# Performance work log

Hardware: AMD Instinct MI355X
Metric: run time of the kernel (lower is better)

## Reference

```python
import jax, jax.numpy as jnp
import numpy as np


def setup_inputs() -> dict:
    key = jax.random.key(0)
    k1, k2 = jax.random.split(key)
    N, I, J, K = 256, 32, 32, 256
    x = jax.random.normal(k1, (N, I, K), dtype=jnp.float32)
    z = jax.random.normal(k2, (N, J, K), dtype=jnp.float32)
    return {"x": x, "z": z}


def reference(x, z):
    # Original torch code loops over batch rolls; rolling only permutes the set
    # over which log_softmax (a permutation-invariant logsumexp) is taken, and
    # index 0 of the roll stack is always the diagonal pair (x[n], z[n]).
    # So it is exactly a symmetric InfoNCE over the full pairwise score matrix.
    J = z.shape[1]
    # Full pairwise token-level similarity: [N_x, N_z, I, J]
    sim = jnp.einsum('aik,bjk->abij', x, z)
    # score(x_a, z_b) = sum_{i,j} softmax_i(sim)*sim / J
    w = jax.nn.softmax(sim, axis=2) * sim
    S = w.sum(axis=(2, 3)) / J  # [N_x, N_z]
    diag = jnp.diagonal(S)
    # loss_x[n] = -log_softmax over x-candidates (axis 0) at the diagonal
    loss_x = jax.nn.logsumexp(S, axis=0) - diag
    # loss_z[n] = -log_softmax over z-candidates (axis 1) at the diagonal
    loss_z = jax.nn.logsumexp(S, axis=1) - diag
    loss = loss_x + loss_z
    return loss.mean()  # reduction='mean'
```

## Files before the change

### kernel.cpp

```cpp
#include <hip/hip_runtime.h>
#include <hip/hip_bf16.h>
#include <hip/hip_fp16.h>
#include <stdint.h>


typedef __attribute__((ext_vector_type(8))) short short8;
typedef __attribute__((ext_vector_type(16))) float float16;
typedef __attribute__((ext_vector_type(8))) int int8v;
typedef __attribute__((ext_vector_type(4))) int int4v;

typedef const __attribute__((address_space(1))) unsigned int* gptr_as1;
typedef __attribute__((address_space(3))) unsigned int* lptr_as3;

#define NTOK 256
#define KDIM 256

__device__ __forceinline__ unsigned short f2bf(float f) {
    unsigned int u = __float_as_uint(f);
    unsigned int r = (u + 0x7fffu + ((u >> 16) & 1u)) >> 16;
    return (unsigned short)r;
}

__device__ __forceinline__ short8 cvt8(const float* p) {
    float4 f0 = ((const float4*)p)[0];
    float4 f1 = ((const float4*)p)[1];
    short8 v;
    v[0] = (short)f2bf(f0.x); v[1] = (short)f2bf(f0.y);
    v[2] = (short)f2bf(f0.z); v[3] = (short)f2bf(f0.w);
    v[4] = (short)f2bf(f1.x); v[5] = (short)f2bf(f1.y);
    v[6] = (short)f2bf(f1.z); v[7] = (short)f2bf(f1.w);
    return v;
}

__global__ void conv_fp8(const float* __restrict__ x,
                         const float* __restrict__ z,
                         int4v* __restrict__ q,
                         float* __restrict__ out0) {
    const int uid = blockIdx.x * 256 + threadIdx.x;
    if (uid == 0) out0[0] = 0.0f;
    const int tensor = uid >> 16;
    const int idx    = uid & 65535;
    const int g    = idx >> 8;
    const int r    = idx & 255;
    const int ks   = r >> 6;
    const int lane = r & 63;
    const int row  = g * 32 + (lane & 31);
    const int k0   = ks * 64 + (lane >> 5) * 32;
    const float4* p = (const float4*)((tensor ? z : x) + row * KDIM + k0);

    int4v lo, hi;
#pragma unroll
    for (int i = 0; i < 4; i++) {
        float4 f = p[i];
        int v = __builtin_amdgcn_cvt_pk_fp8_f32(f.x, f.y, 0, false);
        v = __builtin_amdgcn_cvt_pk_fp8_f32(f.z, f.w, v, true);
        lo[i] = v;
    }
#pragma unroll
    for (int i = 0; i < 4; i++) {
        float4 f = p[4 + i];
        int v = __builtin_amdgcn_cvt_pk_fp8_f32(f.x, f.y, 0, false);
        v = __builtin_amdgcn_cvt_pk_fp8_f32(f.z, f.w, v, true);
        hi[i] = v;
    }
    q[tensor * 131072 + idx]         = lo;
    q[tensor * 131072 + 65536 + idx] = hi;
}

__device__ __forceinline__ int8v mk8(int4v lo, int4v hi) {
    int8v r;
    r[0] = lo[0]; r[1] = lo[1]; r[2] = lo[2]; r[3] = lo[3];
    r[4] = hi[0]; r[5] = hi[1]; r[6] = hi[2]; r[7] = hi[3];
    return r;
}

#define MFMA_FP8(a, b, c) \
    __builtin_amdgcn_mfma_scale_f32_32x32x64_f8f6f4((a), (b), (c), 0, 0, 0, 0x7F7F7F7F, 0, 0x7F7F7F7F)

__device__ __forceinline__ void tile_epilogue_sp(const float16& c, __half* __restrict__ Sp,
                                                 int a, int b, int lane) {
    float m8[8], m4[4];
#pragma unroll
    for (int r = 0; r < 8; r++) m8[r] = fmaxf(c[2 * r], c[2 * r + 1]);
#pragma unroll
    for (int r = 0; r < 4; r++) m4[r] = fmaxf(m8[2 * r], m8[2 * r + 1]);
    float m = fmaxf(fmaxf(m4[0], m4[1]), fmaxf(m4[2], m4[3]));
    m = fmaxf(m, __shfl_xor(m, 32, 64));

    float s0 = 0.f, s1 = 0.f, s2 = 0.f, s3 = 0.f;
    float w0 = 0.f, w1 = 0.f, w2 = 0.f, w3 = 0.f;
#pragma unroll
    for (int r = 0; r < 16; r += 4) {
        float e0 = __expf(c[r + 0] - m);
        float e1 = __expf(c[r + 1] - m);
        float e2 = __expf(c[r + 2] - m);
        float e3 = __expf(c[r + 3] - m);
        s0 += e0; s1 += e1; s2 += e2; s3 += e3;
        w0 = fmaf(e0, c[r + 0], w0);
        w1 = fmaf(e1, c[r + 1], w1);
        w2 = fmaf(e2, c[r + 2], w2);
        w3 = fmaf(e3, c[r + 3], w3);
    }
    float se  = (s0 + s1) + (s2 + s3);
    float swe = (w0 + w1) + (w2 + w3);
    se  += __shfl_xor(se, 32, 64);
    swe += __shfl_xor(swe, 32, 64);
    float cv = swe * __builtin_amdgcn_rcpf(se);
    Sp[(((a << 8) + b) << 6) + lane] = __float2half_rn(cv);
}

__global__ __launch_bounds__(256, 3)
void sim_fp8(const int4v* __restrict__ q, __half* __restrict__ Sp) {
    __shared__ int4v sA[1024];

    const int tid  = threadIdx.x;
    const int lane = tid & 63;
    const int w    = tid >> 6;

    const int apair = blockIdx.x >> 5;
    const int boct  = blockIdx.x & 31;
    const int ag0   = apair * 2;
    const int bg0   = boct * 8 + w * 2;

#pragma unroll
    for (int i = 0; i < 4; i++) {
        const int c  = i * 4 + w;
        const int ai = c >> 3;
        const int ks = (c >> 1) & 3;
        const int h  = c & 1;
        const int4v* g = q + h * 65536 + ((ag0 + ai) * 4 + ks) * 64 + lane;
        int4v* l = &sA[c * 64];
        __builtin_amdgcn_global_load_lds((gptr_as1)g, (lptr_as3)l, 16, 0, 0);
    }
    __syncthreads();

    const int4v* zq = q + 131072;

    float16 acc00, acc01, acc10, acc11;
#pragma unroll
    for (int r = 0; r < 16; r++) { acc00[r] = 0.f; acc01[r] = 0.f; acc10[r] = 0.f; acc11[r] = 0.f; }

#pragma unroll
    for (int ks = 0; ks < 4; ks++) {
        const int u0 = ((bg0 + 0) * 4 + ks) * 64 + lane;
        const int u1 = ((bg0 + 1) * 4 + ks) * 64 + lane;
        int8v Ba = mk8(zq[u0], zq[65536 + u0]);
        int8v Bb = mk8(zq[u1], zq[65536 + u1]);
        const int a0 = (ks * 2) * 64 + lane;
        const int a1 = (8 + ks * 2) * 64 + lane;
        int8v A0 = mk8(sA[a0], sA[a0 + 64]);
        int8v A1 = mk8(sA[a1], sA[a1 + 64]);
        acc00 = MFMA_FP8(A0, Ba, acc00);
        acc01 = MFMA_FP8(A0, Bb, acc01);
        acc10 = MFMA_FP8(A1, Ba, acc10);
        acc11 = MFMA_FP8(A1, Bb, acc11);
    }

    tile_epilogue_sp(acc00, Sp, ag0 + 0, bg0 + 0, lane);
    tile_epilogue_sp(acc01, Sp, ag0 + 0, bg0 + 1, lane);
    tile_epilogue_sp(acc10, Sp, ag0 + 1, bg0 + 0, lane);
    tile_epilogue_sp(acc11, Sp, ag0 + 1, bg0 + 1, lane);
}

__global__ void conv_kernel(const float* __restrict__ x,
                            const float* __restrict__ z,
                            short8* __restrict__ outbf,
                            float* __restrict__ out0) {
    const int uid = blockIdx.x * 256 + threadIdx.x;
    if (uid == 0) out0[0] = 0.0f;
    const int u = uid & 262143;
    const float* src = (uid < 262144) ? x : z;
    const int g  = u >> 10;
    const int r  = u & 1023;
    const int ks = r >> 6;
    const int h  = (r >> 5) & 1;
    const int l  = r & 31;
    outbf[uid] = cvt8(src + ((g * 32 + l) * KDIM + ks * 16 + h * 8));
}

__device__ __forceinline__ void tile_epilogue_bf(const float16& c, float* __restrict__ S,
                                                 int a, int b, int lane) {
    float m8[8], m4[4];
#pragma unroll
    for (int r = 0; r < 8; r++) m8[r] = fmaxf(c[2 * r], c[2 * r + 1]);
#pragma unroll
    for (int r = 0; r < 4; r++) m4[r] = fmaxf(m8[2 * r], m8[2 * r + 1]);
    float m = fmaxf(fmaxf(m4[0], m4[1]), fmaxf(m4[2], m4[3]));
    m = fmaxf(m, __shfl_xor(m, 32, 64));

    float s0 = 0.f, s1 = 0.f, s2 = 0.f, s3 = 0.f;
    float w0 = 0.f, w1 = 0.f, w2 = 0.f, w3 = 0.f;
#pragma unroll
    for (int r = 0; r < 16; r += 4) {
        float e0 = __expf(c[r + 0] - m);
        float e1 = __expf(c[r + 1] - m);
        float e2 = __expf(c[r + 2] - m);
        float e3 = __expf(c[r + 3] - m);
        s0 += e0; s1 += e1; s2 += e2; s3 += e3;
        w0 = fmaf(e0, c[r + 0], w0);
        w1 = fmaf(e1, c[r + 1], w1);
        w2 = fmaf(e2, c[r + 2], w2);
        w3 = fmaf(e3, c[r + 3], w3);
    }
    float se  = (s0 + s1) + (s2 + s3);
    float swe = (w0 + w1) + (w2 + w3);
    se  += __shfl_xor(se, 32, 64);
    swe += __shfl_xor(swe, 32, 64);
    float cv = swe * __builtin_amdgcn_rcpf(se);
#pragma unroll
    for (int off = 1; off < 32; off <<= 1) cv += __shfl_xor(cv, off, 64);
    if (lane == 0) S[a * NTOK + b] = cv * (1.0f / 32.0f);
}

#define MFMA_BF16 __builtin_amdgcn_mfma_f32_32x32x16_bf16

template <bool F32SRC>
__global__ __launch_bounds__(256, 2)
void sim_kernel(const short8* __restrict__ xbf, const short8* __restrict__ zbf,
                const float* __restrict__ xf, const float* __restrict__ zf,
                float* __restrict__ S) {
    __shared__ short8 sA[4096];

    const int tid  = threadIdx.x;
    const int lane = tid & 63;
    const int w    = tid >> 6;
    const int l31  = lane & 31;
    const int half = lane >> 5;

    const int ablk = blockIdx.x >> 5;
    const int bblk = blockIdx.x & 31;
    const int ag0  = ablk * 4;
    const int bg0  = bblk * 8 + w * 2;

    float16 acc[4][2];
#pragma unroll
    for (int ai = 0; ai < 4; ai++)
#pragma unroll
        for (int bi = 0; bi < 2; bi++)
#pragma unroll
            for (int r = 0; r < 16; r++) acc[ai][bi][r] = 0.0f;

    if (!F32SRC) {
        const short8* asrc = xbf + (size_t)ablk * 4096;
#pragma unroll
        for (int i = 0; i < 16; i++) {
            const short8* g = asrc + i * 256 + w * 64 + lane;
            short8* l = &sA[i * 256 + w * 64];
            __builtin_amdgcn_global_load_lds((gptr_as1)g, (lptr_as3)l, 16, 0, 0);
        }
        __syncthreads();

        const short8* pb0 = zbf + (bg0 + 0) * 1024 + lane;
        const short8* pb1 = zbf + (bg0 + 1) * 1024 + lane;
        short8 Ba = pb0[0];
        short8 Bb = pb1[0];
#pragma unroll
        for (int ks = 0; ks < 16; ks++) {
            short8 Na, Nb;
            if (ks < 15) { Na = pb0[(ks + 1) * 64]; Nb = pb1[(ks + 1) * 64]; }
            short8 A0 = sA[ks * 64 + lane];
            short8 A1 = sA[1024 + ks * 64 + lane];
            short8 A2 = sA[2048 + ks * 64 + lane];
            short8 A3 = sA[3072 + ks * 64 + lane];
            acc[0][0] = MFMA_BF16(A0, Ba, acc[0][0], 0, 0, 0);
            acc[0][1] = MFMA_BF16(A0, Bb, acc[0][1], 0, 0, 0);
            acc[1][0] = MFMA_BF16(A1, Ba, acc[1][0], 0, 0, 0);
            acc[1][1] = MFMA_BF16(A1, Bb, acc[1][1], 0, 0, 0);
            acc[2][0] = MFMA_BF16(A2, Ba, acc[2][0], 0, 0, 0);
            acc[2][1] = MFMA_BF16(A2, Bb, acc[2][1], 0, 0, 0);
            acc[3][0] = MFMA_BF16(A3, Ba, acc[3][0], 0, 0, 0);
            acc[3][1] = MFMA_BF16(A3, Bb, acc[3][1], 0, 0, 0);
            Ba = Na; Bb = Nb;
        }
    } else {
        const float* fb0 = zf + (((bg0 + 0) * 32 + l31) * KDIM + half * 8);
        const float* fb1 = zf + (((bg0 + 1) * 32 + l31) * KDIM + half * 8);
#pragma unroll 1
        for (int ks = 0; ks < 16; ks++) {
            short8 Ba = cvt8(fb0 + ks * 16);
            short8 Bb = cvt8(fb1 + ks * 16);
#pragma unroll
            for (int ai = 0; ai < 4; ai++) {
                const float* fa = xf + (((ag0 + ai) * 32 + l31) * KDIM + half * 8);
                short8 Af = cvt8(fa + ks * 16);
                acc[ai][0] = MFMA_BF16(Af, Ba, acc[ai][0], 0, 0, 0);
                acc[ai][1] = MFMA_BF16(Af, Bb, acc[ai][1], 0, 0, 0);
            }
        }
    }

#pragma unroll
    for (int ai = 0; ai < 4; ai++)
#pragma unroll
        for (int bi = 0; bi < 2; bi++)
            tile_epilogue_bf(acc[ai][bi], S, ag0 + ai, bg0 + bi, lane);
}

__global__ void red_kernel(const __half* __restrict__ Sp, float* __restrict__ S) {
    const int t = blockIdx.x * 256 + threadIdx.x;
    const __half2* h2 = (const __half2*)(Sp + (size_t)t * 64);
    float s = 0.0f;
#pragma unroll
    for (int i = 0; i < 32; i++) {
        float2 f = __half22float2(h2[i]);
        s += f.x + f.y;
    }
    S[t] = s * (1.0f / 64.0f);
}

__global__ void loss_part(const float* __restrict__ S, float* __restrict__ out) {
    const int lane = threadIdx.x & 63;
    const int wid  = threadIdx.x >> 6;
    const int n    = blockIdx.x * 4 + wid;

    float cv[4], rv[4];
#pragma unroll
    for (int k = 0; k < 4; k++) {
        const int t = lane + 64 * k;
        cv[k] = S[t * NTOK + n];
        rv[k] = S[n * NTOK + t];
    }
    float m = fmaxf(fmaxf(cv[0], cv[1]), fmaxf(cv[2], cv[3]));
#pragma unroll
    for (int off = 1; off < 64; off <<= 1) m = fmaxf(m, __shfl_xor(m, off, 64));
    float s = 0.0f;
#pragma unroll
    for (int k = 0; k < 4; k++) s += __expf(cv[k] - m);
#pragma unroll
    for (int off = 1; off < 64; off <<= 1) s += __shfl_xor(s, off, 64);
    float lse_col = m + __logf(s);

    float m2 = fmaxf(fmaxf(rv[0], rv[1]), fmaxf(rv[2], rv[3]));
#pragma unroll
    for (int off = 1; off < 64; off <<= 1) m2 = fmaxf(m2, __shfl_xor(m2, off, 64));
    float s2 = 0.0f;
#pragma unroll
    for (int k = 0; k < 4; k++) s2 += __expf(rv[k] - m2);
#pragma unroll
    for (int off = 1; off < 64; off <<= 1) s2 += __shfl_xor(s2, off, 64);
    float lse_row = m2 + __logf(s2);

    __shared__ float red[4];
    if (lane == 0) {
        float diag = S[n * NTOK + n];
        red[wid] = (lse_col - diag) + (lse_row - diag);
    }
    __syncthreads();
    if (threadIdx.x == 0)
        atomicAdd(out, (red[0] + red[1] + red[2] + red[3]) * (1.0f / 256.0f));
}

__global__ void zero_kernel(float* __restrict__ out) {
    out[0] = 0.0f;
}

extern "C" void kernel_launch(void* const* d_in, const int* in_sizes, int n_in,
                              void* d_out, int out_size, void* d_ws, size_t ws_size,
                              hipStream_t stream) {
    const float* x = (const float*)d_in[0];
    const float* z = (const float*)d_in[1];
    float* out = (float*)d_out;

    const size_t q_bytes  = 262144ull * 16ull;
    const size_t sp_bytes = 65536ull * 64ull * 2ull;
    const size_t s_bytes  = 256ull * 256ull * 4ull;
    const size_t bf_bytes = 524288ull * 16ull;

    if (ws_size >= q_bytes + sp_bytes + s_bytes) {
        int4v*  q  = (int4v*)d_ws;
        __half* Sp = (__half*)((char*)d_ws + q_bytes);
        float*  S  = (float*)((char*)d_ws + q_bytes + sp_bytes);
        conv_fp8<<<512, 256, 0, stream>>>(x, z, q, out);
        sim_fp8<<<4096, 256, 0, stream>>>(q, Sp);
        red_kernel<<<256, 256, 0, stream>>>(Sp, S);
        loss_part<<<64, 256, 0, stream>>>(S, out);
    } else if (ws_size >= bf_bytes + s_bytes) {
        short8* xbf = (short8*)d_ws;
        short8* zbf = xbf + 262144;
        float*  S   = (float*)((char*)d_ws + bf_bytes);
        conv_kernel<<<2048, 256, 0, stream>>>(x, z, (short8*)d_ws, out);
        sim_kernel<false><<<2048, 256, 0, stream>>>(xbf, zbf, nullptr, nullptr, S);
        loss_part<<<64, 256, 0, stream>>>(S, out);
    } else {
        float* S = (float*)d_ws;
        zero_kernel<<<1, 1, 0, stream>>>(out);
        sim_kernel<true><<<2048, 256, 0, stream>>>(nullptr, nullptr, x, z, S);
        loss_part<<<64, 256, 0, stream>>>(S, out);
    }
}
```

Measured before the change: 98.09 us.

## Fuse reduction into loss kernel and loop sim_fp8 over more b-tiles per block

The sim_fp8 kernel now runs 1024 blocks, each looping over four b-pairs per wave, so the A tile staged in LDS is reused across more z tiles and fewer blocks are launched. The per-tile epilogue is interleaved across four accumulators to expose more ILP in the exp/shuffle chain. The separate red_kernel and loss_part are replaced by one loss_fused kernel that sums the half partials per row and per column directly and atomically accumulates the loss. This removes one launch and the intermediate S buffer, but each partial is now read twice, and the column reads are strided.

```diff
diff --git a/kernel.cpp b/kernel.cpp
--- a/kernel.cpp
+++ b/kernel.cpp
@@ -77,36 +77,47 @@
 #define MFMA_FP8(a, b, c) \
     __builtin_amdgcn_mfma_scale_f32_32x32x64_f8f6f4((a), (b), (c), 0, 0, 0, 0x7F7F7F7F, 0, 0x7F7F7F7F)
 
-__device__ __forceinline__ void tile_epilogue_sp(const float16& c, __half* __restrict__ Sp,
-                                                 int a, int b, int lane) {
+__device__ __forceinline__ float tile_max(const float16& c) {
     float m8[8], m4[4];
 #pragma unroll
     for (int r = 0; r < 8; r++) m8[r] = fmaxf(c[2 * r], c[2 * r + 1]);
 #pragma unroll
     for (int r = 0; r < 4; r++) m4[r] = fmaxf(m8[2 * r], m8[2 * r + 1]);
-    float m = fmaxf(fmaxf(m4[0], m4[1]), fmaxf(m4[2], m4[3]));
-    m = fmaxf(m, __shfl_xor(m, 32, 64));
+    return fmaxf(fmaxf(m4[0], m4[1]), fmaxf(m4[2], m4[3]));
+}
+
+__device__ __forceinline__ void epilogue4(const float16& c0, const float16& c1,
+                                          const float16& c2, const float16& c3,
+                                          __half* __restrict__ Sp,
+                                          int ag0, int bg, int lane) {
+    float m0 = tile_max(c0), m1 = tile_max(c1), m2 = tile_max(c2), m3 = tile_max(c3);
+    m0 = fmaxf(m0, __shfl_xor(m0, 32, 64));
+    m1 = fmaxf(m1, __shfl_xor(m1, 32, 64));
+    m2 = fmaxf(m2, __shfl_xor(m2, 32, 64));
+    m3 = fmaxf(m3, __shfl_xor(m3, 32, 64));
 
     float s0 = 0.f, s1 = 0.f, s2 = 0.f, s3 = 0.f;
     float w0 = 0.f, w1 = 0.f, w2 = 0.f, w3 = 0.f;
 #pragma unroll
-    for (int r = 0; r < 16; r += 4) {
-        float e0 = __expf(c[r + 0] - m);
-        float e1 = __expf(c[r + 1] - m);
-        float e2 = __expf(c[r + 2] - m);
-        float e3 = __expf(c[r + 3] - m);
-        s0 += e0; s1 += e1; s2 += e2; s3 += e3;
-        w0 = fmaf(e0, c[r + 0], w0);
-        w1 = fmaf(e1, c[r + 1], w1);
-        w2 = fmaf(e2, c[r + 2], w2);
-        w3 = fmaf(e3, c[r + 3], w3);
-    }
-    float se  = (s0 + s1) + (s2 + s3);
-    float swe = (w0 + w1) + (w2 + w3);
-    se  += __shfl_xor(se, 32, 64);
-    swe += __shfl_xor(swe, 32, 64);
-    float cv = swe * __builtin_amdgcn_rcpf(se);
-    Sp[(((a << 8) + b) << 6) + lane] = __float2half_rn(cv);
+    for (int r = 0; r < 16; r++) {
+        float e0 = __expf(c0[r] - m0); s0 += e0; w0 = fmaf(e0, c0[r], w0);
+        float e1 = __expf(c1[r] - m1); s1 += e1; w1 = fmaf(e1, c1[r], w1);
+        float e2 = __expf(c2[r] - m2); s2 += e2; w2 = fmaf(e2, c2[r], w2);
+        float e3 = __expf(c3[r] - m3); s3 += e3; w3 = fmaf(e3, c3[r], w3);
+    }
+
+    s0 += __shfl_xor(s0, 32, 64); w0 += __shfl_xor(w0, 32, 64);
+    s1 += __shfl_xor(s1, 32, 64); w1 += __shfl_xor(w1, 32, 64);
+    s2 += __shfl_xor(s2, 32, 64); w2 += __shfl_xor(w2, 32, 64);
+    s3 += __shfl_xor(s3, 32, 64); w3 += __shfl_xor(w3, 32, 64);
+    float v0 = w0 * __builtin_amdgcn_rcpf(s0);
+    float v1 = w1 * __builtin_amdgcn_rcpf(s1);
+    float v2 = w2 * __builtin_amdgcn_rcpf(s2);
+    float v3 = w3 * __builtin_amdgcn_rcpf(s3);
+    Sp[((((ag0 + 0) << 8) + bg + 0) << 6) + lane] = __float2half_rn(v0);
+    Sp[((((ag0 + 0) << 8) + bg + 1) << 6) + lane] = __float2half_rn(v1);
+    Sp[((((ag0 + 1) << 8) + bg + 0) << 6) + lane] = __float2half_rn(v2);
+    Sp[((((ag0 + 1) << 8) + bg + 1) << 6) + lane] = __float2half_rn(v3);
 }
 
 __global__ __launch_bounds__(256, 3)
@@ -117,10 +128,10 @@
     const int lane = tid & 63;
     const int w    = tid >> 6;
 
-    const int apair = blockIdx.x >> 5;
-    const int boct  = blockIdx.x & 31;
-    const int ag0   = apair * 2;
-    const int bg0   = boct * 8 + w * 2;
+    const int apair  = blockIdx.x >> 3;
+    const int brange = blockIdx.x & 7;
+    const int ag0    = apair * 2;
+    const int bbase  = brange * 32 + w * 8;
 
 #pragma unroll
     for (int i = 0; i < 4; i++) {
@@ -136,30 +147,87 @@
 
     const int4v* zq = q + 131072;
 
-    float16 acc00, acc01, acc10, acc11;
-#pragma unroll
-    for (int r = 0; r < 16; r++) { acc00[r] = 0.f; acc01[r] = 0.f; acc10[r] = 0.f; acc11[r] = 0.f; }
-
-#pragma unroll
-    for (int ks = 0; ks < 4; ks++) {
-        const int u0 = ((bg0 + 0) * 4 + ks) * 64 + lane;
-        const int u1 = ((bg0 + 1) * 4 + ks) * 64 + lane;
-        int8v Ba = mk8(zq[u0], zq[65536 + u0]);
-        int8v Bb = mk8(zq[u1], zq[65536 + u1]);
-        const int a0 = (ks * 2) * 64 + lane;
-        const int a1 = (8 + ks * 2) * 64 + lane;
-        int8v A0 = mk8(sA[a0], sA[a0 + 64]);
-        int8v A1 = mk8(sA[a1], sA[a1 + 64]);
-        acc00 = MFMA_FP8(A0, Ba, acc00);
-        acc01 = MFMA_FP8(A0, Bb, acc01);
-        acc10 = MFMA_FP8(A1, Ba, acc10);
-        acc11 = MFMA_FP8(A1, Bb, acc11);
-    }
-
-    tile_epilogue_sp(acc00, Sp, ag0 + 0, bg0 + 0, lane);
-    tile_epilogue_sp(acc01, Sp, ag0 + 0, bg0 + 1, lane);
-    tile_epilogue_sp(acc10, Sp, ag0 + 1, bg0 + 0, lane);
-    tile_epilogue_sp(acc11, Sp, ag0 + 1, bg0 + 1, lane);
+#pragma unroll 1
+    for (int p = 0; p < 4; p++) {
+        const int bg = bbase + 2 * p;
+
+        float16 acc00, acc01, acc10, acc11;
+#pragma unroll
+        for (int r = 0; r < 16; r++) { acc00[r] = 0.f; acc01[r] = 0.f; acc10[r] = 0.f; acc11[r] = 0.f; }
+
+#pragma unroll
+        for (int ks = 0; ks < 4; ks++) {
+            const int u0 = ((bg + 0) * 4 + ks) * 64 + lane;
+            const int u1 = ((bg + 1) * 4 + ks) * 64 + lane;
+            int8v Ba = mk8(zq[u0], zq[65536 + u0]);
+            int8v Bb = mk8(zq[u1], zq[65536 + u1]);
+            const int a0 = (ks * 2) * 64 + lane;
+            const int a1 = (8 + ks * 2) * 64 + lane;
+            int8v A0 = mk8(sA[a0], sA[a0 + 64]);
+            int8v A1 = mk8(sA[a1], sA[a1 + 64]);
+            acc00 = MFMA_FP8(A0, Ba, acc00);
+            acc01 = MFMA_FP8(A0, Bb, acc01);
+            acc10 = MFMA_FP8(A1, Ba, acc10);
+            acc11 = MFMA_FP8(A1, Bb, acc11);
+        }
+
+        epilogue4(acc00, acc01, acc10, acc11, Sp, ag0, bg, lane);
+    }
+}
+
+__global__ void loss_fused(const __half* __restrict__ Sp, float* __restrict__ out) {
+    const int n    = blockIdx.x;
+    const int k    = threadIdx.x;
+    const int lane = k & 63;
+    const int wv   = k >> 6;
+
+    const __half2* rp = (const __half2*)(Sp + ((size_t)(n * 256 + k) << 6));
+    const __half2* cp = (const __half2*)(Sp + ((size_t)(k * 256 + n) << 6));
+    float rs = 0.f, cs = 0.f;
+#pragma unroll
+    for (int i = 0; i < 32; i++) {
+        float2 f = __half22float2(rp[i]);
+        rs += f.x + f.y;
+    }
+#pragma unroll
+    for (int i = 0; i < 32; i++) {
+        float2 f = __half22float2(cp[i]);
+        cs += f.x + f.y;
+    }
+    rs *= (1.0f / 64.0f);
+    cs *= (1.0f / 64.0f);
+
+    __shared__ float shm[8];
+    __shared__ float shs[8];
+    __shared__ float sdiag;
+    if (k == n) sdiag = rs;
+
+    float mr = rs, mc = cs;
+#pragma unroll
+    for (int off = 1; off < 64; off <<= 1) {
+        mr = fmaxf(mr, __shfl_xor(mr, off, 64));
+        mc = fmaxf(mc, __shfl_xor(mc, off, 64));
+    }
+    if (lane == 0) { shm[wv] = mr; shm[4 + wv] = mc; }
+    __syncthreads();
+    mr = fmaxf(fmaxf(shm[0], shm[1]), fmaxf(shm[2], shm[3]));
+    mc = fmaxf(fmaxf(shm[4], shm[5]), fmaxf(shm[6], shm[7]));
+
+    float er = __expf(rs - mr), ec = __expf(cs - mc);
+#pragma unroll
+    for (int off = 1; off < 64; off <<= 1) {
+        er += __shfl_xor(er, off, 64);
+        ec += __shfl_xor(ec, off, 64);
+    }
+    if (lane == 0) { shs[wv] = er; shs[4 + wv] = ec; }
+    __syncthreads();
+    if (k == 0) {
+        float sr = (shs[0] + shs[1]) + (shs[2] + shs[3]);
+        float sc = (shs[4] + shs[5]) + (shs[6] + shs[7]);
+        float lse_row = mr + __logf(sr);
+        float lse_col = mc + __logf(sc);
+        atomicAdd(out, (lse_row + lse_col - 2.0f * sdiag) * (1.0f / 256.0f));
+    }
 }
 
 __global__ void conv_kernel(const float* __restrict__ x,
@@ -180,12 +248,7 @@
 
 __device__ __forceinline__ void tile_epilogue_bf(const float16& c, float* __restrict__ S,
                                                  int a, int b, int lane) {
-    float m8[8], m4[4];
-#pragma unroll
-    for (int r = 0; r < 8; r++) m8[r] = fmaxf(c[2 * r], c[2 * r + 1]);
-#pragma unroll
-    for (int r = 0; r < 4; r++) m4[r] = fmaxf(m8[2 * r], m8[2 * r + 1]);
-    float m = fmaxf(fmaxf(m4[0], m4[1]), fmaxf(m4[2], m4[3]));
+    float m = tile_max(c);
     m = fmaxf(m, __shfl_xor(m, 32, 64));
 
     float s0 = 0.f, s1 = 0.f, s2 = 0.f, s3 = 0.f;
@@ -296,18 +359,6 @@
             tile_epilogue_bf(acc[ai][bi], S, ag0 + ai, bg0 + bi, lane);
 }
 
-__global__ void red_kernel(const __half* __restrict__ Sp, float* __restrict__ S) {
-    const int t = blockIdx.x * 256 + threadIdx.x;
-    const __half2* h2 = (const __half2*)(Sp + (size_t)t * 64);
-    float s = 0.0f;
-#pragma unroll
-    for (int i = 0; i < 32; i++) {
-        float2 f = __half22float2(h2[i]);
-        s += f.x + f.y;
-    }
-    S[t] = s * (1.0f / 64.0f);
-}
-
 __global__ void loss_part(const float* __restrict__ S, float* __restrict__ out) {
     const int lane = threadIdx.x & 63;
     const int wid  = threadIdx.x >> 6;
@@ -366,14 +417,12 @@
     const size_t s_bytes  = 256ull * 256ull * 4ull;
     const size_t bf_bytes = 524288ull * 16ull;
 
-    if (ws_size >= q_bytes + sp_bytes + s_bytes) {
+    if (ws_size >= q_bytes + sp_bytes) {
         int4v*  q  = (int4v*)d_ws;
         __half* Sp = (__half*)((char*)d_ws + q_bytes);
-        float*  S  = (float*)((char*)d_ws + q_bytes + sp_bytes);
         conv_fp8<<<512, 256, 0, stream>>>(x, z, q, out);
-        sim_fp8<<<4096, 256, 0, stream>>>(q, Sp);
-        red_kernel<<<256, 256, 0, stream>>>(Sp, S);
-        loss_part<<<64, 256, 0, stream>>>(S, out);
+        sim_fp8<<<1024, 256, 0, stream>>>(q, Sp);
+        loss_fused<<<256, 256, 0, stream>>>(Sp, out);
     } else if (ws_size >= bf_bytes + s_bytes) {
         short8* xbf = (short8*)d_ws;
         short8* zbf = xbf + 262144;
```

New measurement: 100.6 us. 2.5% more time.
